# Optimization experiments

Measured on AMD Instinct MI355X. Metric: run time of the kernel, lower is better.

Reference implementation:

```python
import jax, jax.numpy as jnp
import numpy as np
from jax import lax

B, C, OUT, H, W = 8, 512, 512, 64, 64
BN_EPS = 1e-5


def setup_inputs() -> dict:
    key = jax.random.key(0)
    ks = jax.random.split(key, 20)
    s = 1.0 / np.sqrt(C)
    d = {
        "input1": jax.random.normal(ks[0], (B, C, H, W), jnp.float32),
        "input2": jax.random.normal(ks[1], (B, C, H, W), jnp.float32),
        "wq1": jax.random.normal(ks[2], (C, C), jnp.float32) * s,
        "bq1": jnp.zeros((C,), jnp.float32),
        "wk1": jax.random.normal(ks[3], (C, C), jnp.float32) * s,
        "bk1": jnp.zeros((C,), jnp.float32),
        "wv1": jax.random.normal(ks[4], (C, C), jnp.float32) * s,
        "bv1": jnp.zeros((C,), jnp.float32),
        "wq2": jax.random.normal(ks[5], (C, C), jnp.float32) * s,
        "bq2": jnp.zeros((C,), jnp.float32),
        "wk2": jax.random.normal(ks[6], (C, C), jnp.float32) * s,
        "bk2": jnp.zeros((C,), jnp.float32),
        "wv2": jax.random.normal(ks[7], (C, C), jnp.float32) * s,
        "bv2": jnp.zeros((C,), jnp.float32),
        "w_lin": jax.random.normal(ks[8], (1, C), jnp.float32) * s,  # shared gate conv, no bias
        "w_cat": jax.random.normal(ks[9], (OUT, 2 * C, 3, 3), jnp.float32) * (1.0 / np.sqrt(2 * C * 9)),
        "bn_gamma": jnp.ones((OUT,), jnp.float32),
        "bn_beta": jnp.zeros((OUT,), jnp.float32),
    }
    return d


def _conv1x1(x, w, b):
    # x: [B,C,H,W], w: [O,C] -> [B,O,H,W]
    return jnp.einsum('bchw,oc->bohw', x, w) + b[None, :, None, None]


def _branch(x_q_src, x_kv_src, wq, bq, wk, bk, wv, bv, w_lin, x_resid):
    # matches: attn = softmax(k(x_kv) @ q(x_q)^T); out = attn^T @ v(x_kv)
    b, c, h, w = x_kv_src.shape
    n = h * w
    q = _conv1x1(x_q_src, wq, bq).reshape(b, c, n)      # [B,C,N] (from the OTHER input)
    k = _conv1x1(x_kv_src, wk, bk).reshape(b, c, n)
    v = _conv1x1(x_kv_src, wv, bv).reshape(b, c, n)
    attn = jnp.einsum('bkn,bcn->bkc', k, q)             # [B,C,C]
    attn = jax.nn.softmax(attn, axis=-1)
    out = jnp.einsum('bkc,bkn->bcn', attn, v).reshape(b, c, h, w)
    # sigmoid gate: linear(avgpool(x_resid)) -> scalar per batch
    pooled = jnp.mean(x_resid, axis=(2, 3))             # [B,C]
    a = jax.nn.sigmoid(pooled @ w_lin.T)                # [B,1]
    return out * a[:, :, None, None] + x_resid


def reference(input1, input2, wq1, bq1, wk1, bk1, wv1, bv1,
              wq2, bq2, wk2, bk2, wv2, bv2, w_lin, w_cat, bn_gamma, bn_beta):
    # branch 1: k1 from input1, q2 from input2, v1 from input1, gate from input1
    out1 = _branch(input2, input1, wq2, bq2, wk1, bk1, wv1, bv1, w_lin, input1)
    # branch 2: k2 from input2, q1 from input1, v2 from input2, gate from input2
    out2 = _branch(input1, input2, wq1, bq1, wk2, bk2, wv2, bv2, w_lin, input2)
    x = jnp.concatenate([out1, out2], axis=1)           # [B,2C,H,W]
    y = lax.conv_general_dilated(x, w_cat, (1, 1), 'SAME',
                                 dimension_numbers=('NCHW', 'OIHW', 'NCHW'))
    # BatchNorm2d in training mode: batch statistics over (N,H,W)
    mean = jnp.mean(y, axis=(0, 2, 3), keepdims=True)
    var = jnp.var(y, axis=(0, 2, 3), keepdims=True)
    y = (y - mean) * lax.rsqrt(var + BN_EPS)
    y = y * bn_gamma[None, :, None, None] + bn_beta[None, :, None, None]
    return jax.nn.relu(y)
```

## Files before the change

kernel.cpp:

```cpp
#include <hip/hip_runtime.h>


typedef unsigned short u16;
typedef unsigned int u32;
typedef float f32x4 __attribute__((ext_vector_type(4)));
typedef short bf16x8 __attribute__((ext_vector_type(8)));

#define DEV __device__ __forceinline__

DEV u16 f2bf(float f) {
  u32 u = __float_as_uint(f);
  return (u16)((u + 0x7fffu + ((u >> 16) & 1u)) >> 16);
}
DEV float bf2f(u16 u) { return __uint_as_float(((u32)u) << 16); }

DEV void gload_lds16(const void* g, void* l) {
  __builtin_amdgcn_global_load_lds(
      (const __attribute__((address_space(1))) void*)g,
      (__attribute__((address_space(3))) void*)l, 16, 0, 0);
}

DEV void stage_tile(u16* L, const u16* src, int row0, long ld, int k0, int wid, int lane) {
  int rr = lane >> 2;
  int cc = (lane & 3) << 3;
#pragma unroll
  for (int j = 0; j < 2; ++j) {
    int chunk = j * 4 + wid;
    const u16* g = src + (long)(row0 + chunk * 16 + rr) * ld + (k0 + cc);
    gload_lds16(g, L + chunk * 512);
  }
}

DEV float waveRedSum(float v) {
#pragma unroll
  for (int o = 32; o > 0; o >>= 1) v += __shfl_xor(v, o);
  return v;
}

DEV float blockReduceSum256(float v) {
  __shared__ float r[4];
  v = waveRedSum(v);
  int tid = threadIdx.x;
  if ((tid & 63) == 0) r[tid >> 6] = v;
  __syncthreads();
  return r[0] + r[1] + r[2] + r[3];
}

__global__ __launch_bounds__(256) void gemm_gramK(const float* __restrict__ X1,
                                                  const float* __restrict__ X2,
                                                  float* __restrict__ parts)
{
  __shared__ __align__(16) u16 lds[4 * 4096];
  const int bid = blockIdx.x;
  const int cid = ((bid & 7) << 6) + (bid >> 3);
  const int z = cid >> 4, xy = cid & 15;
  const int quarter = z >> 3, b = z & 7;
  const int m0 = (xy & 3) * 128, n0 = (xy >> 2) * 128;
  const int tid = threadIdx.x, wid = tid >> 6, lane = tid & 63;
  const int wr = wid >> 1, wc = wid & 1;
  const int r16 = lane & 15, koff = (lane >> 4) << 3;
  const float* A = X1 + (long)b * 2097152 + quarter * 1024;
  const float* Bp = X2 + (long)b * 2097152 + quarter * 1024;
  const int sr = tid >> 3;
  const int sc = (tid & 7) * 4;

  f32x4 acc[4][4];
#pragma unroll
  for (int i = 0; i < 4; ++i)
#pragma unroll
    for (int j = 0; j < 4; ++j) acc[i][j] = (f32x4){0.f, 0.f, 0.f, 0.f};

  for (int k0 = 0; k0 < 1024; k0 += 32) {
    __syncthreads();
#pragma unroll
    for (int rr = 0; rr < 128; rr += 32) {
      float4 va = *(const float4*)&A[(long)(m0 + rr + sr) * 4096 + k0 + sc];
      float4 vb = *(const float4*)&Bp[(long)(n0 + rr + sr) * 4096 + k0 + sc];
      float fa[4] = {va.x, va.y, va.z, va.w};
      float fb[4] = {vb.x, vb.y, vb.z, vb.w};
      u32 pah0 = 0, pah1 = 0, pal0 = 0, pal1 = 0;
      u32 pbh0 = 0, pbh1 = 0, pbl0 = 0, pbl1 = 0;
#pragma unroll
      for (int e = 0; e < 2; ++e) {
        u16 h = f2bf(fa[e]);      pah0 |= ((u32)h) << (16 * e);
        u16 lo = f2bf(fa[e] - bf2f(h)); pal0 |= ((u32)lo) << (16 * e);
        h = f2bf(fa[e + 2]);      pah1 |= ((u32)h) << (16 * e);
        lo = f2bf(fa[e + 2] - bf2f(h)); pal1 |= ((u32)lo) << (16 * e);
        h = f2bf(fb[e]);          pbh0 |= ((u32)h) << (16 * e);
        lo = f2bf(fb[e] - bf2f(h)); pbl0 |= ((u32)lo) << (16 * e);
        h = f2bf(fb[e + 2]);      pbh1 |= ((u32)h) << (16 * e);
        lo = f2bf(fb[e + 2] - bf2f(h)); pbl1 |= ((u32)lo) << (16 * e);
      }
      int off = (rr + sr) * 32 + sc;
      *(uint2*)&lds[off]         = make_uint2(pah0, pah1);
      *(uint2*)&lds[4096 + off]  = make_uint2(pal0, pal1);
      *(uint2*)&lds[8192 + off]  = make_uint2(pbh0, pbh1);
      *(uint2*)&lds[12288 + off] = make_uint2(pbl0, pbl1);
    }
    __syncthreads();
    bf16x8 ah[4], al[4], bh[4], bl[4];
#pragma unroll
    for (int mi = 0; mi < 4; ++mi) {
      ah[mi] = *(const bf16x8*)&lds[(wr * 64 + mi * 16 + r16) * 32 + koff];
      al[mi] = *(const bf16x8*)&lds[4096 + (wr * 64 + mi * 16 + r16) * 32 + koff];
    }
#pragma unroll
    for (int nj = 0; nj < 4; ++nj) {
      bh[nj] = *(const bf16x8*)&lds[8192 + (wc * 64 + nj * 16 + r16) * 32 + koff];
      bl[nj] = *(const bf16x8*)&lds[12288 + (wc * 64 + nj * 16 + r16) * 32 + koff];
    }
#pragma unroll
    for (int mi = 0; mi < 4; ++mi)
#pragma unroll
      for (int nj = 0; nj < 4; ++nj) {
        acc[mi][nj] = __builtin_amdgcn_mfma_f32_16x16x32_bf16(ah[mi], bh[nj], acc[mi][nj], 0, 0, 0);
        acc[mi][nj] = __builtin_amdgcn_mfma_f32_16x16x32_bf16(ah[mi], bl[nj], acc[mi][nj], 0, 0, 0);
        acc[mi][nj] = __builtin_amdgcn_mfma_f32_16x16x32_bf16(al[mi], bh[nj], acc[mi][nj], 0, 0, 0);
      }
  }

  const int rq = lane >> 4;
  float* O = parts + (long)z * 262144;
#pragma unroll
  for (int mi = 0; mi < 4; ++mi)
#pragma unroll
    for (int nj = 0; nj < 4; ++nj)
#pragma unroll
      for (int i = 0; i < 4; ++i) {
        int row = m0 + wr * 64 + mi * 16 + rq * 4 + i;
        int col = n0 + wc * 64 + nj * 16 + r16;
        O[(long)row * 512 + col] = acc[mi][nj][i];
      }
}

__global__ __launch_bounds__(256) void k_gsplit(const float* __restrict__ parts,
                                                u16* __restrict__ Gh, u16* __restrict__ Gl)
{
  for (long i = (long)blockIdx.x * 256 + threadIdx.x; i < 2097152; i += (long)gridDim.x * 256) {
    float v = parts[i] + parts[i + 2097152] + parts[i + 4194304] + parts[i + 6291456];
    u16 h = f2bf(v);
    Gh[i] = h;
    Gl[i] = f2bf(v - bf2f(h));
  }
}

constexpr int EP_SPLIT = 0, EP_LOGITS = 1, EP_BF16 = 2, EP_XCAT = 3;

struct GArgs {
  const u16* Ah[2]; const u16* Al[2];
  const u16* Bh[2]; const u16* Bl[2];
  long Az[2], Bz[2];
  void* O0[2]; void* O1[2];
  const float* f0[2]; const float* f1[2];
  const float* f2[2]; const float* f3[2];
  const u16* rptr[2];
};

template <int EP, bool SPLIT3, bool FLAT>
__global__ __launch_bounds__(256) void gemm_tn2(GArgs ga, int lda, int ldb, int K, long Oz)
{
  __shared__ __align__(16) u16 lds[(SPLIT3 ? 4 : 2) * 4096];
  int bx, by, z;
  if constexpr (FLAT) {
    const int cid = ((blockIdx.x & 7) << 8) + (blockIdx.x >> 3);
    z = cid >> 7;
    const int xy = cid & 127;
    bx = xy >> 2; by = xy & 3;
  } else {
    bx = blockIdx.x; by = blockIdx.y; z = blockIdx.z;
  }
  const int br = z >> 3, b = z & 7;
  const u16* pAh = ga.Ah[br] + (long)b * ga.Az[br];
  const u16* pBh = ga.Bh[br] + (long)b * ga.Bz[br];
  const u16* pAl = SPLIT3 ? ga.Al[br] + (long)b * ga.Az[br] : nullptr;
  const u16* pBl = SPLIT3 ? ga.Bl[br] + (long)b * ga.Bz[br] : nullptr;
  const int m0 = bx * 128, n0 = by * 128;
  const int tid = threadIdx.x, wid = tid >> 6, lane = tid & 63;
  const int wr = wid >> 1, wc = wid & 1;
  const int r16 = lane & 15, koff = (lane >> 4) << 3;

  f32x4 acc[4][4];
#pragma unroll
  for (int i = 0; i < 4; ++i)
#pragma unroll
    for (int j = 0; j < 4; ++j) acc[i][j] = (f32x4){0.f, 0.f, 0.f, 0.f};

  for (int k0 = 0; k0 < K; k0 += 32) {
    __syncthreads();
    stage_tile(lds, pAh, m0, lda, k0, wid, lane);
    stage_tile(lds + 4096, pBh, n0, ldb, k0, wid, lane);
    if constexpr (SPLIT3) {
      stage_tile(lds + 8192, pAl, m0, lda, k0, wid, lane);
      stage_tile(lds + 12288, pBl, n0, ldb, k0, wid, lane);
    }
    __syncthreads();
    bf16x8 af[4], bfh[4], af2[4], bf2_[4];
#pragma unroll
    for (int mi = 0; mi < 4; ++mi)
      af[mi] = *(const bf16x8*)&lds[(wr * 64 + mi * 16 + r16) * 32 + koff];
#pragma unroll
    for (int nj = 0; nj < 4; ++nj)
      bfh[nj] = *(const bf16x8*)&lds[4096 + (wc * 64 + nj * 16 + r16) * 32 + koff];
    if constexpr (SPLIT3) {
#pragma unroll
      for (int mi = 0; mi < 4; ++mi)
        af2[mi] = *(const bf16x8*)&lds[8192 + (wr * 64 + mi * 16 + r16) * 32 + koff];
#pragma unroll
      for (int nj = 0; nj < 4; ++nj)
        bf2_[nj] = *(const bf16x8*)&lds[12288 + (wc * 64 + nj * 16 + r16) * 32 + koff];
    }
#pragma unroll
    for (int mi = 0; mi < 4; ++mi)
#pragma unroll
      for (int nj = 0; nj < 4; ++nj) {
        acc[mi][nj] = __builtin_amdgcn_mfma_f32_16x16x32_bf16(af[mi], bfh[nj], acc[mi][nj], 0, 0, 0);
        if constexpr (SPLIT3) {
          acc[mi][nj] = __builtin_amdgcn_mfma_f32_16x16x32_bf16(af[mi], bf2_[nj], acc[mi][nj], 0, 0, 0);
          acc[mi][nj] = __builtin_amdgcn_mfma_f32_16x16x32_bf16(af2[mi], bfh[nj], acc[mi][nj], 0, 0, 0);
        }
      }
  }

  const int rq = lane >> 4;
  const long off = (long)z * Oz;
  float g = 0.f;
  if constexpr (EP == EP_XCAT) g = ga.f1[br][b];
#pragma unroll
  for (int mi = 0; mi < 4; ++mi)
#pragma unroll
    for (int nj = 0; nj < 4; ++nj)
#pragma unroll
      for (int i = 0; i < 4; ++i) {
        int row = m0 + wr * 64 + mi * 16 + rq * 4 + i;
        int col = n0 + wc * 64 + nj * 16 + r16;
        float v = acc[mi][nj][i];
        if constexpr (EP == EP_SPLIT) {
          long idx = off + (long)row * 512 + col;
          u16 h = f2bf(v);
          ((u16*)ga.O0[br])[idx] = h;
          ((u16*)ga.O1[br])[idx] = f2bf(v - bf2f(h));
        } else if constexpr (EP == EP_LOGITS) {
          v += ga.f0[br][row] * ga.f3[br][b * 512 + col] + ga.f1[br][col] * ga.f2[br][b * 512 + row];
          ((float*)ga.O0[br])[off + (long)row * 512 + col] = v;
        } else if constexpr (EP == EP_BF16) {
          ((u16*)ga.O0[br])[off + (long)row * 512 + col] = f2bf(v);
        } else {
          float val = (v + ga.f0[br][b * 512 + col]) * g +
                      bf2f(ga.rptr[br][(long)b * 2097152 + (long)row * 512 + col]);
          int yy = row >> 6, xx = row & 63;
          long oidx = ((long)(b * 66 + yy + 1) * 66 + (xx + 1)) * 512 + col;
          ((u16*)ga.O0[br])[oidx] = f2bf(val);
        }
      }
}

#define MF(a, b, c) __builtin_amdgcn_mfma_f32_16x16x32_bf16(a, b, c, 0, 0, 0)
#define SCHEDB() __builtin_amdgcn_sched_barrier(0)
#define BAR() __builtin_amdgcn_s_barrier()
#define STG_B(QB, i) gload_lds16(xb + sbo[i] + kko, &lds[(QB) + ldsB0 + (i) * 4096])
#define STG_A(QB, i) gload_lds16(Arow + (i) * 294912L + Aoff, &lds[(QB) + ldsA0 + (i) * 2048])

#define RD_A(d, fmb)                                                        \
  d##0 = *(const bf16x8*)&lds[pBase + aRd + (fmb) * 1024 + sxa0];           \
  d##1 = *(const bf16x8*)&lds[pBase + aRd + (fmb) * 1024 + sxa1];           \
  d##2 = *(const bf16x8*)&lds[pBase + aRd + ((fmb) + 1) * 1024 + sxa0];     \
  d##3 = *(const bf16x8*)&lds[pBase + aRd + ((fmb) + 1) * 1024 + sxa1];

#define MM(jj, r)                                                           \
  __builtin_amdgcn_s_setprio(1);                                            \
  _Pragma("unroll")                                                         \
  for (int fn = 0; fn < 4; ++fn) {                                          \
    acc[2 * (jj)][fn] = MF(r##0, bq[fn][0], acc[2 * (jj)][fn]);             \
    acc[2 * (jj)][fn] = MF(r##1, bq[fn][1], acc[2 * (jj)][fn]);             \
    acc[2 * (jj) + 1][fn] = MF(r##2, bq[fn][0], acc[2 * (jj) + 1][fn]);     \
    acc[2 * (jj) + 1][fn] = MF(r##3, bq[fn][1], acc[2 * (jj) + 1][fn]);     \
  }                                                                         \
  __builtin_amdgcn_s_setprio(0);                                            \
  SCHEDB();

__global__ __launch_bounds__(512, 2) void k_conv8(const u16* __restrict__ W,
                                                  const u16* __restrict__ xA,
                                                  const u16* __restrict__ xB,
                                                  float* __restrict__ y,
                                                  float* __restrict__ bnsum,
                                                  float* __restrict__ bnsum2)
{
  __shared__ __align__(16) u16 lds[65536];
  const int cid = ((blockIdx.x & 7) << 5) + (blockIdx.x >> 3);
  const int bz = cid >> 5, mx = (cid >> 4) & 1, ny = cid & 15;
  const int m0 = mx * 256, n0 = ny * 256;
  const long zoff = (long)bz * 2230272;

  const int tid = threadIdx.x;
  const int w = tid >> 6, l = tid & 63;
  const int wr = w >> 2, wcn = w & 3, wl = w & 3;
  const int lr = l >> 3, l7 = l & 7, l15 = l & 15, l4 = l >> 4;
  const int ss8 = (l7 ^ lr) << 3;

  long sbo[4];
#pragma unroll
  for (int i = 0; i < 4; ++i) {
    int n = n0 + i * 64 + w * 8 + lr;
    sbo[i] = (long)((n >> 6) * 66 + (n & 63)) * 512;
  }
  const u16* Arow = W + (long)(m0 + wr * 128 + wl * 8 + lr) * 9216 + ss8;
  const int ldsA0 = wr * 8192 + wl * 512;
  const int ldsB0 = 16384 + w * 512;
  const int sxa0 = (l4 ^ l7) << 3;
  const int sxa1 = ((l4 | 4) ^ l7) << 3;
  const int aRd = wr * 8192 + l15 * 64;
  const int bRd = 16384 + wcn * 4096 + l15 * 64;

  f32x4 acc[8][4];
#pragma unroll
  for (int i = 0; i < 8; ++i)
#pragma unroll
    for (int j = 0; j < 4; ++j) acc[i][j] = (f32x4){0.f, 0.f, 0.f, 0.f};

  {
    const u16* xb = xA + zoff;
    const long kko = ss8;
    const long Aoff = 0;
    STG_B(0, 0); STG_B(0, 1); STG_B(0, 2); STG_B(0, 3);
    STG_A(0, 0); STG_A(0, 1); STG_A(0, 2); STG_A(0, 3);
  }

  for (int t = 0; t < 144; ++t) {
    const int pBase = (t & 1) << 15;
    const int qBase = pBase ^ 32768;
    const int tau = t + 1;
    const bool pf = tau < 144;
    const int ccc = tau / 9;
    const int tap = tau - ccc * 9;
    const int cch = ccc << 6;
    const u16* xb = ((cch & 512) ? xB : xA) + zoff;
    const long kko = (long)((tap / 3) * 66 + (tap % 3)) * 512 + (cch & 511) + ss8;
    const long Aoff = (long)(tap << 10) + cch;
    bf16x8 bq[4][2];
    bf16x8 cA0, cA1, cA2, cA3, nA0, nA1, nA2, nA3;

    if (pf) { STG_B(qBase, 0); STG_B(qBase, 1); asm volatile("s_waitcnt vmcnt(4)" ::: "memory"); }
    else    { asm volatile("s_waitcnt vmcnt(2)" ::: "memory"); }
    BAR(); SCHEDB();
#pragma unroll
    for (int fn = 0; fn < 4; ++fn) {
      bq[fn][0] = *(const bf16x8*)&lds[pBase + bRd + fn * 1024 + sxa0];
      bq[fn][1] = *(const bf16x8*)&lds[pBase + bRd + fn * 1024 + sxa1];
    }
    RD_A(cA, 0)
    RD_A(nA, 2)
    SCHEDB();
    MM(0, cA)
    if (pf) { STG_B(qBase, 2); STG_B(qBase, 3); asm volatile("s_waitcnt vmcnt(5)" ::: "memory"); }
    else    { asm volatile("s_waitcnt vmcnt(1)" ::: "memory"); }
    BAR(); SCHEDB();
    RD_A(cA, 4)
    SCHEDB();
    MM(1, nA)
    if (pf) { STG_A(qBase, 0); STG_A(qBase, 1); asm volatile("s_waitcnt vmcnt(6)" ::: "memory"); }
    else    { asm volatile("s_waitcnt vmcnt(0)" ::: "memory"); }
    BAR(); SCHEDB();
    RD_A(nA, 6)
    SCHEDB();
    MM(2, cA)
    if (pf) { STG_A(qBase, 2); STG_A(qBase, 3); }
    BAR(); SCHEDB();
    MM(3, nA)
  }

#pragma unroll
  for (int fm = 0; fm < 8; ++fm)
#pragma unroll
    for (int fn = 0; fn < 4; ++fn)
#pragma unroll
      for (int i = 0; i < 4; ++i) {
        int row = m0 + wr * 128 + fm * 16 + l4 * 4 + i;
        int col = n0 + wcn * 64 + fn * 16 + l15;
        y[((long)bz * 512 + row) * 4096 + col] = acc[fm][fn][i];
      }

  __syncthreads();
  float* fl = (float*)lds;
#pragma unroll
  for (int fm = 0; fm < 8; ++fm)
#pragma unroll
    for (int i = 0; i < 4; ++i) {
      float s = acc[fm][0][i] + acc[fm][1][i] + acc[fm][2][i] + acc[fm][3][i];
      float s2 = acc[fm][0][i] * acc[fm][0][i] + acc[fm][1][i] * acc[fm][1][i] +
                 acc[fm][2][i] * acc[fm][2][i] + acc[fm][3][i] * acc[fm][3][i];
#pragma unroll
      for (int m = 1; m < 16; m <<= 1) { s += __shfl_xor(s, m); s2 += __shfl_xor(s2, m); }
      if (l15 == 0) {
        int r = wr * 128 + fm * 16 + l4 * 4 + i;
        fl[r * 4 + wcn] = s;
        fl[1024 + r * 4 + wcn] = s2;
      }
    }
  __syncthreads();
  {
    int r = tid & 255;
    int which = tid >> 8;
    const float* p = fl + which * 1024 + r * 4;
    float v = p[0] + p[1] + p[2] + p[3];
    atomicAdd((which ? bnsum2 : bnsum) + m0 + r, v);
  }
}

__global__ __launch_bounds__(256) void k_border(u16* __restrict__ xcat, float* __restrict__ rsum,
                                                float* __restrict__ bnsum)
{
  const long base = (long)blockIdx.x * 2230272;
  const int tid = threadIdx.x;
  const uint4 z4 = make_uint4(0, 0, 0, 0);
  for (int i = tid; i < 8448; i += 256) {
    long off = (i < 4224) ? (long)i * 8 : (long)65 * 66 * 512 + (long)(i - 4224) * 8;
    *(uint4*)&xcat[base + off] = z4;
  }
  for (int i = tid; i < 8192; i += 256) {
    int y = 1 + (i >> 7);
    int xsel = (i >> 6) & 1;
    int v = i & 63;
    long off = ((long)y * 66 + (xsel ? 65 : 0)) * 512 + (long)v * 8;
    *(uint4*)&xcat[base + off] = z4;
  }
  float4 f4 = {0.f, 0.f, 0.f, 0.f};
  if (blockIdx.x == 0) {
    for (int i = tid; i < 2048; i += 256) ((float4*)rsum)[i] = f4;
  } else if (blockIdx.x == 1) {
    for (int i = tid; i < 256; i += 256) ((float4*)bnsum)[i] = f4;
  }
}

__global__ __launch_bounds__(256) void k_prep(const float* __restrict__ src,
                                              u16* __restrict__ xT, float* __restrict__ rsum)
{
  __shared__ float t[64][65];
  const int b = blockIdx.z, cb = blockIdx.y, nb = blockIdx.x;
  const float* s = src + (long)b * 2097152;
  const int tid = threadIdx.x;
#pragma unroll
  for (int it = 0; it < 4; ++it) {
    int cr = it * 16 + (tid >> 4);
    int nc = (tid & 15) * 4;
    float4 v = *(const float4*)&s[(long)(cb * 64 + cr) * 4096 + nb * 64 + nc];
    t[cr][nc] = v.x; t[cr][nc + 1] = v.y; t[cr][nc + 2] = v.z; t[cr][nc + 3] = v.w;
  }
  __syncthreads();
  int nr = tid >> 2, cs = (tid & 3) * 16;
  u16 hh[16] __attribute__((aligned(16)));
#pragma unroll
  for (int j = 0; j < 16; ++j) hh[j] = f2bf(t[cs + j][nr]);
  long d = (long)b * 2097152 + (long)(nb * 64 + nr) * 512 + cb * 64 + cs;
  *(uint4*)&xT[d] = *(const uint4*)&hh[0];
  *(uint4*)&xT[d + 8] = *(const uint4*)&hh[8];
  if (tid < 64) {
    float sum = 0.f;
#pragma unroll 8
    for (int j = 0; j < 64; ++j) sum += t[tid][j];
    atomicAdd(&rsum[b * 512 + cb * 64 + tid], sum);
  }
}

__global__ __launch_bounds__(256) void k_tr(const float* __restrict__ src, u16* __restrict__ dst,
                                            int scols, int srows, long zsrc, long zdst)
{
  __shared__ float t[64][65];
  src += (long)blockIdx.z * zsrc;
  dst += (long)blockIdx.z * zdst;
  const int c0 = blockIdx.x * 64, r0 = blockIdx.y * 64;
  const int tid = threadIdx.x;
#pragma unroll
  for (int it = 0; it < 4; ++it) {
    int rr = it * 16 + (tid >> 4);
    int cc = (tid & 15) * 4;
    float4 v = *(const float4*)&src[(long)(r0 + rr) * scols + c0 + cc];
    t[rr][cc] = v.x; t[rr][cc + 1] = v.y; t[rr][cc + 2] = v.z; t[rr][cc + 3] = v.w;
  }
  __syncthreads();
  int nr = tid >> 2, cs = (tid & 3) * 16;
  u16 hh[16] __attribute__((aligned(16)));
#pragma unroll
  for (int j = 0; j < 16; ++j) hh[j] = f2bf(t[cs + j][nr]);
  long d = (long)(c0 + nr) * srows + r0 + cs;
  *(uint4*)&dst[d] = *(const uint4*)&hh[0];
  *(uint4*)&dst[d + 8] = *(const uint4*)&hh[8];
}

__global__ __launch_bounds__(256) void k_gate(const float* __restrict__ rowsum,
                                              const float* __restrict__ wlin,
                                              float* __restrict__ gates)
{
  int id = blockIdx.x;
  int inp = id >> 3, b = id & 7;
  int tid = threadIdx.x;
  float s = 0.f;
  for (int c = tid; c < 512; c += 256) s += rowsum[inp * 4096 + b * 512 + c] * wlin[c];
  s = blockReduceSum256(s);
  if (tid == 0) gates[id] = 1.f / (1.f + __expf(-s / 4096.f));
}

__global__ __launch_bounds__(256) void k_skq(const float* __restrict__ wk1, const float* __restrict__ wq2,
                                             const float* __restrict__ wk2, const float* __restrict__ wq1,
                                             const float* __restrict__ bq2, const float* __restrict__ bq1,
                                             const float* __restrict__ rowsum, float* __restrict__ S)
{
  int which = blockIdx.y, b = blockIdx.z;
  int row = blockIdx.x * 4 + (threadIdx.x >> 6);
  int lane = threadIdx.x & 63;
  const float* W; const float* rs; const float* bias = nullptr;
  if (which == 0)      { W = wk1; rs = rowsum + b * 512; }
  else if (which == 1) { W = wq2; rs = rowsum + 4096 + b * 512; bias = bq2; }
  else if (which == 2) { W = wk2; rs = rowsum + 4096 + b * 512; }
  else                 { W = wq1; rs = rowsum + b * 512; bias = bq1; }
  float s = 0.f;
  for (int i = lane; i < 512; i += 64) s += W[row * 512 + i] * rs[i];
  s = waveRedSum(s);
  if (lane == 0) S[(which * 8 + b) * 512 + row] = s + (bias ? 4096.f * bias[row] : 0.f);
}

__global__ __launch_bounds__(256) void k_mbias(const u16* __restrict__ attnT,
                                               const float* __restrict__ bv1,
                                               const float* __restrict__ bv2,
                                               float* __restrict__ mb)
{
  int z = blockIdx.y;
  int c = blockIdx.x * 4 + (threadIdx.x >> 6);
  int lane = threadIdx.x & 63;
  const float* bv = (z >= 8) ? bv2 : bv1;
  const u16* row = attnT + (long)z * 262144 + (long)c * 512;
  float s = 0.f;
  for (int k = lane; k < 512; k += 64) s += bf2f(row[k]) * bv[k];
  s = waveRedSum(s);
  if (lane == 0) mb[z * 512 + c] = s;
}

struct SplitArgs { const float* s[4]; u16* h[4]; u16* l[4]; };
__global__ __launch_bounds__(256) void k_split4(SplitArgs a)
{
  int which = blockIdx.x >> 8;
  const float* s = a.s[which];
  u16* h = a.h[which];
  u16* l = a.l[which];
  for (int i = (blockIdx.x & 255) * 256 + threadIdx.x; i < 262144; i += 65536) {
    float v = s[i];
    u16 hh = f2bf(v);
    h[i] = hh;
    l[i] = f2bf(v - bf2f(hh));
  }
}

__global__ __launch_bounds__(256) void k_wcat(const float* __restrict__ src, u16* __restrict__ dst)
{
  __shared__ float t[9 * 1029];
  const int o = blockIdx.x;
  const int tid = threadIdx.x;
  const float* s = src + (long)o * 9216;
#pragma unroll
  for (int it = 0; it < 9; ++it) {
    int f4 = it * 256 + tid;
    float4 v = *(const float4*)&s[f4 * 4];
    float va[4] = {v.x, v.y, v.z, v.w};
    int f = f4 * 4;
#pragma unroll
    for (int e = 0; e < 4; ++e) {
      int ic = (f + e) / 9, tp = (f + e) - ic * 9;
      t[tp * 1029 + ic] = va[e];
    }
  }
  __syncthreads();
  u16* d = dst + (long)o * 9216;
#pragma unroll
  for (int tp = 0; tp < 9; ++tp)
#pragma unroll
    for (int c = 0; c < 4; ++c) {
      int ic = c * 256 + tid;
      d[tp * 1024 + ic] = f2bf(t[tp * 1029 + ic]);
    }
}

__global__ __launch_bounds__(256) void k_softmaxT(const float* __restrict__ L,
                                                  u16* __restrict__ attnT)
{
  const int bid = blockIdx.x;
  const int z = bid >> 4, rg = bid & 15;
  const int w = threadIdx.x >> 6, lane = threadIdx.x & 63;
  const int a0 = rg * 32 + w * 8;
  const float* Lz = L + (long)z * 262144;
  u16* Az = attnT + (long)z * 262144;
  u32 pk[8][4] = {};
#pragma unroll
  for (int it = 0; it < 8; ++it) {
    long base = (long)(a0 + it) * 512 + lane * 8;
    float4 p0 = *(const float4*)&Lz[base], p1 = *(const float4*)&Lz[base + 4];
    float v[8] = {p0.x, p0.y, p0.z, p0.w, p1.x, p1.y, p1.z, p1.w};
    float m = v[0];
#pragma unroll
    for (int j = 1; j < 8; ++j) m = fmaxf(m, v[j]);
#pragma unroll
    for (int o = 32; o > 0; o >>= 1) m = fmaxf(m, __shfl_xor(m, o));
    float e[8], s = 0.f;
#pragma unroll
    for (int j = 0; j < 8; ++j) { e[j] = __expf(v[j] - m); s += e[j]; }
    s = waveRedSum(s);
    float inv = 1.f / s;
#pragma unroll
    for (int j = 0; j < 8; ++j)
      pk[j][it >> 1] |= ((u32)f2bf(e[j] * inv)) << ((it & 1) * 16);
  }
#pragma unroll
  for (int j = 0; j < 8; ++j) {
    int c = lane * 8 + j;
    *(uint4*)&Az[(long)c * 512 + a0] = make_uint4(pk[j][0], pk[j][1], pk[j][2], pk[j][3]);
  }
}

__global__ __launch_bounds__(512) void k_bnstat(const float* __restrict__ bnsum,
                                                const float* __restrict__ bnsum2,
                                                const float* __restrict__ gamma,
                                                const float* __restrict__ beta,
                                                float* __restrict__ sc, float* __restrict__ sh)
{
  int o = threadIdx.x;
  float mean = bnsum[o] / 32768.f;
  float var = bnsum2[o] / 32768.f - mean * mean;
  float rstd = rsqrtf(var + 1e-5f);
  float scale = gamma[o] * rstd;
  sc[o] = scale;
  sh[o] = beta[o] - mean * scale;
}

__global__ __launch_bounds__(256) void k_bnapply(float* __restrict__ y,
                                                 const float* __restrict__ sc,
                                                 const float* __restrict__ sh)
{
  const long n = 16777216;
  for (long i = ((long)blockIdx.x * 256 + threadIdx.x) * 4; i < n; i += (long)gridDim.x * 1024) {
    float4 v = *(const float4*)&y[i];
    int o = (int)((i >> 12) & 511);
    float a = sc[o], c = sh[o];
    v.x = fmaxf(v.x * a + c, 0.f);
    v.y = fmaxf(v.y * a + c, 0.f);
    v.z = fmaxf(v.z * a + c, 0.f);
    v.w = fmaxf(v.w * a + c, 0.f);
    *(float4*)&y[i] = v;
  }
}

extern "C" void kernel_launch(void* const* d_in, const int* in_sizes, int n_in,
                              void* d_out, int out_size, void* d_ws, size_t ws_size,
                              hipStream_t stream)
{
  (void)in_sizes; (void)n_in; (void)out_size; (void)ws_size;
  const float* in1 = (const float*)d_in[0];
  const float* in2 = (const float*)d_in[1];
  const float* wq1 = (const float*)d_in[2];  const float* bq1 = (const float*)d_in[3];
  const float* wk1 = (const float*)d_in[4];  const float* bk1 = (const float*)d_in[5];
  const float* wv1 = (const float*)d_in[6];  const float* bv1 = (const float*)d_in[7];
  const float* wq2 = (const float*)d_in[8];  const float* bq2 = (const float*)d_in[9];
  const float* wk2 = (const float*)d_in[10]; const float* bk2 = (const float*)d_in[11];
  const float* wv2 = (const float*)d_in[12]; const float* bv2 = (const float*)d_in[13];
  const float* wlin  = (const float*)d_in[14];
  const float* wcat  = (const float*)d_in[15];
  const float* gamma = (const float*)d_in[16];
  const float* beta  = (const float*)d_in[17];

  char* ws = (char*)d_ws;
  const size_t MB = 1024ull * 1024ull;
  u16* Gh     = (u16*)(ws + 0 * MB);
  u16* Gl     = (u16*)(ws + 4 * MB);
  u16* Mb     = (u16*)(ws + 0 * MB);
  u16* Uh     = (u16*)(ws + 8 * MB);
  u16* attnT  = (u16*)(ws + 8 * MB);
  u16* Ul     = (u16*)(ws + 16 * MB);
  float* logits = (float*)(ws + 24 * MB);
  float* parts  = (float*)(ws + 8 * MB);
  u16* xcatA  = (u16*)(ws + 40 * MB);
  u16* xcatB  = xcatA + 8L * 2230272;
  u16* wcp    = (u16*)(ws + 112 * MB);
  u16* wsp    = (u16*)(ws + 122 * MB);
  u16* WvT1   = (u16*)(ws + 126 * MB);
  u16* WvT2   = WvT1 + 262144;
  float* rowsum = (float*)(ws + 127 * MB);
  float* gates  = (float*)(ws + 127 * MB + 32 * 1024);
  float* S      = (float*)(ws + 127 * MB + 36 * 1024);
  float* mb     = (float*)(ws + 127 * MB + 100 * 1024);
  float* bnsum  = (float*)(ws + 127 * MB + 132 * 1024);
  float* bnsum2 = (float*)(ws + 127 * MB + 134 * 1024);
  float* bnsc   = (float*)(ws + 127 * MB + 136 * 1024);
  float* bnsh   = (float*)(ws + 127 * MB + 138 * 1024);

  u16* wq1h = wsp + 0 * 262144; u16* wq1l = wsp + 1 * 262144;
  u16* wq2h = wsp + 2 * 262144; u16* wq2l = wsp + 3 * 262144;
  u16* wk1h = wsp + 4 * 262144; u16* wk1l = wsp + 5 * 262144;
  u16* wk2h = wsp + 6 * 262144; u16* wk2l = wsp + 7 * 262144;

  u16* xT1 = (u16*)d_out;
  u16* xT2 = (u16*)d_out + 16777216;
  float* ybuf = (float*)d_out;

  k_border<<<16, 256, 0, stream>>>(xcatA, rowsum, bnsum);
  k_prep<<<dim3(64, 8, 8), 256, 0, stream>>>(in1, xT1, rowsum);
  k_prep<<<dim3(64, 8, 8), 256, 0, stream>>>(in2, xT2, rowsum + 4096);
  k_tr<<<dim3(8, 8, 1), 256, 0, stream>>>(wv1, WvT1, 512, 512, 0L, 0L);
  k_tr<<<dim3(8, 8, 1), 256, 0, stream>>>(wv2, WvT2, 512, 512, 0L, 0L);
  {
    SplitArgs sa;
    sa.s[0] = wq1; sa.h[0] = wq1h; sa.l[0] = wq1l;
    sa.s[1] = wq2; sa.h[1] = wq2h; sa.l[1] = wq2l;
    sa.s[2] = wk1; sa.h[2] = wk1h; sa.l[2] = wk1l;
    sa.s[3] = wk2; sa.h[3] = wk2h; sa.l[3] = wk2l;
    k_split4<<<1024, 256, 0, stream>>>(sa);
  }
  k_wcat<<<512, 256, 0, stream>>>(wcat, wcp);
  k_gate<<<16, 256, 0, stream>>>(rowsum, wlin, gates);
  k_skq<<<dim3(128, 4, 8), 256, 0, stream>>>(wk1, wq2, wk2, wq1, bq2, bq1, rowsum, S);

  gemm_gramK<<<512, 256, 0, stream>>>(in1, in2, parts);
  k_gsplit<<<2048, 256, 0, stream>>>(parts, Gh, Gl);

  {
    GArgs ga = {};
    ga.Ah[0] = wq2h; ga.Al[0] = wq2l; ga.Ah[1] = wk2h; ga.Al[1] = wk2l;
    ga.Az[0] = 0; ga.Az[1] = 0;
    ga.Bh[0] = Gh; ga.Bl[0] = Gl; ga.Bh[1] = Gh; ga.Bl[1] = Gl;
    ga.Bz[0] = 262144; ga.Bz[1] = 262144;
    ga.O0[0] = Uh; ga.O0[1] = Uh; ga.O1[0] = Ul; ga.O1[1] = Ul;
    gemm_tn2<EP_SPLIT, true, false><<<dim3(4, 4, 16), 256, 0, stream>>>(ga, 512, 512, 512, 262144);
  }
  {
    GArgs ga = {};
    ga.Ah[0] = wk1h; ga.Al[0] = wk1l; ga.Az[0] = 0;
    ga.Ah[1] = Uh + 2097152; ga.Al[1] = Ul + 2097152; ga.Az[1] = 262144;
    ga.Bh[0] = Uh; ga.Bl[0] = Ul; ga.Bz[0] = 262144;
    ga.Bh[1] = wq1h; ga.Bl[1] = wq1l; ga.Bz[1] = 0;
    ga.O0[0] = logits; ga.O0[1] = logits;
    ga.f0[0] = bk1; ga.f1[0] = bq2; ga.f2[0] = S;        ga.f3[0] = S + 4096;
    ga.f0[1] = bk2; ga.f1[1] = bq1; ga.f2[1] = S + 8192; ga.f3[1] = S + 12288;
    gemm_tn2<EP_LOGITS, true, false><<<dim3(4, 4, 16), 256, 0, stream>>>(ga, 512, 512, 512, 262144);
  }
  k_softmaxT<<<256, 256, 0, stream>>>(logits, attnT);
  k_mbias<<<dim3(128, 16), 256, 0, stream>>>(attnT, bv1, bv2, mb);
  {
    GArgs ga = {};
    ga.Ah[0] = attnT; ga.Ah[1] = attnT + 2097152;
    ga.Az[0] = 262144; ga.Az[1] = 262144;
    ga.Bh[0] = WvT1; ga.Bh[1] = WvT2; ga.Bz[0] = 0; ga.Bz[1] = 0;
    ga.O0[0] = Mb; ga.O0[1] = Mb;
    gemm_tn2<EP_BF16, false, false><<<dim3(4, 4, 16), 256, 0, stream>>>(ga, 512, 512, 512, 262144);
  }
  {
    GArgs ga = {};
    ga.Ah[0] = xT1; ga.Ah[1] = xT2; ga.Az[0] = 2097152; ga.Az[1] = 2097152;
    ga.Bh[0] = Mb; ga.Bh[1] = Mb + 2097152; ga.Bz[0] = 262144; ga.Bz[1] = 262144;
    ga.O0[0] = xcatA; ga.O0[1] = xcatB;
    ga.f0[0] = mb; ga.f0[1] = mb + 4096;
    ga.f1[0] = gates; ga.f1[1] = gates + 8;
    ga.rptr[0] = xT1; ga.rptr[1] = xT2;
    gemm_tn2<EP_XCAT, false, true><<<2048, 256, 0, stream>>>(ga, 512, 512, 512, 0);
  }

  k_conv8<<<256, 512, 0, stream>>>(wcp, xcatA, xcatB, ybuf, bnsum, bnsum2);
  k_bnstat<<<1, 512, 0, stream>>>(bnsum, bnsum2, gamma, beta, bnsc, bnsh);
  k_bnapply<<<4096, 256, 0, stream>>>(ybuf, bnsc, bnsh);
}
```

Baseline: 613.6 us.

## Merge small prep, gate, mbias and BN-stat kernels to cut launches

Several small setup kernels (border zeroing, Wv transpose, weight split, wcat repack, accumulator zeroing) are merged into one multi-role kernel, and the two input prep launches become one. The gate goes into k_skq, the mbias reduction into softmax through atomics, and BN scale/shift is recomputed inside bnapply. Some SCHEDB barriers are also dropped from the conv loop. This removes about seven launches and their serialization gaps, at the cost of atomics in softmax and redundant per-element BN stat math.

Result: faster. 601.2 us (-2.0%).

```diff
diff --git a/kernel.cpp b/kernel.cpp
--- a/kernel.cpp
+++ b/kernel.cpp
@@ -35,15 +35,6 @@
 #pragma unroll
   for (int o = 32; o > 0; o >>= 1) v += __shfl_xor(v, o);
   return v;
-}
-
-DEV float blockReduceSum256(float v) {
-  __shared__ float r[4];
-  v = waveRedSum(v);
-  int tid = threadIdx.x;
-  if ((tid & 63) == 0) r[tid >> 6] = v;
-  __syncthreads();
-  return r[0] + r[1] + r[2] + r[3];
 }
 
 __global__ __launch_bounds__(256) void gemm_gramK(const float* __restrict__ X1,
@@ -349,19 +340,16 @@
     }
     RD_A(cA, 0)
     RD_A(nA, 2)
-    SCHEDB();
     MM(0, cA)
     if (pf) { STG_B(qBase, 2); STG_B(qBase, 3); asm volatile("s_waitcnt vmcnt(5)" ::: "memory"); }
     else    { asm volatile("s_waitcnt vmcnt(1)" ::: "memory"); }
     BAR(); SCHEDB();
     RD_A(cA, 4)
-    SCHEDB();
     MM(1, nA)
     if (pf) { STG_A(qBase, 0); STG_A(qBase, 1); asm volatile("s_waitcnt vmcnt(6)" ::: "memory"); }
     else    { asm volatile("s_waitcnt vmcnt(0)" ::: "memory"); }
     BAR(); SCHEDB();
     RD_A(nA, 6)
-    SCHEDB();
     MM(2, cA)
     if (pf) { STG_A(qBase, 2); STG_A(qBase, 3); }
     BAR(); SCHEDB();
@@ -406,37 +394,110 @@
   }
 }
 
-__global__ __launch_bounds__(256) void k_border(u16* __restrict__ xcat, float* __restrict__ rsum,
-                                                float* __restrict__ bnsum)
-{
-  const long base = (long)blockIdx.x * 2230272;
+struct PrepArgs {
+  const float* wv1; const float* wv2;
+  u16* WvT1; u16* WvT2;
+  const float* s[4]; u16* h[4]; u16* l[4];
+  const float* wcat; u16* wcp;
+  u16* xcat;
+  float* rsum; float* bnsum; float* mbz;
+};
+
+__global__ __launch_bounds__(256) void k_mprep(PrepArgs a)
+{
+  __shared__ __align__(16) float shbuf[9261];
+  const int bx = blockIdx.x;
   const int tid = threadIdx.x;
-  const uint4 z4 = make_uint4(0, 0, 0, 0);
-  for (int i = tid; i < 8448; i += 256) {
-    long off = (i < 4224) ? (long)i * 8 : (long)65 * 66 * 512 + (long)(i - 4224) * 8;
-    *(uint4*)&xcat[base + off] = z4;
-  }
-  for (int i = tid; i < 8192; i += 256) {
-    int y = 1 + (i >> 7);
-    int xsel = (i >> 6) & 1;
-    int v = i & 63;
-    long off = ((long)y * 66 + (xsel ? 65 : 0)) * 512 + (long)v * 8;
-    *(uint4*)&xcat[base + off] = z4;
-  }
-  float4 f4 = {0.f, 0.f, 0.f, 0.f};
-  if (blockIdx.x == 0) {
-    for (int i = tid; i < 2048; i += 256) ((float4*)rsum)[i] = f4;
-  } else if (blockIdx.x == 1) {
-    for (int i = tid; i < 256; i += 256) ((float4*)bnsum)[i] = f4;
-  }
-}
-
-__global__ __launch_bounds__(256) void k_prep(const float* __restrict__ src,
-                                              u16* __restrict__ xT, float* __restrict__ rsum)
+  if (bx < 128) {
+    const float* src = (bx < 64) ? a.wv1 : a.wv2;
+    u16* dst = (bx < 64) ? a.WvT1 : a.WvT2;
+    const int t8 = bx & 63;
+    const int c0 = (t8 & 7) * 64, r0 = (t8 >> 3) * 64;
+#pragma unroll
+    for (int it = 0; it < 4; ++it) {
+      int rr = it * 16 + (tid >> 4);
+      int cc = (tid & 15) * 4;
+      float4 v = *(const float4*)&src[(long)(r0 + rr) * 512 + c0 + cc];
+      shbuf[rr * 65 + cc] = v.x; shbuf[rr * 65 + cc + 1] = v.y;
+      shbuf[rr * 65 + cc + 2] = v.z; shbuf[rr * 65 + cc + 3] = v.w;
+    }
+    __syncthreads();
+    int nr = tid >> 2, cs = (tid & 3) * 16;
+    u16 hh[16] __attribute__((aligned(16)));
+#pragma unroll
+    for (int j = 0; j < 16; ++j) hh[j] = f2bf(shbuf[(cs + j) * 65 + nr]);
+    long d = (long)(c0 + nr) * 512 + r0 + cs;
+    *(uint4*)&dst[d] = *(const uint4*)&hh[0];
+    *(uint4*)&dst[d + 8] = *(const uint4*)&hh[8];
+  } else if (bx < 1152) {
+    int which = (bx - 128) >> 8;
+    const float* s = a.s[which];
+    u16* h = a.h[which];
+    u16* l = a.l[which];
+    for (int i = ((bx - 128) & 255) * 256 + tid; i < 262144; i += 65536) {
+      float v = s[i];
+      u16 hh = f2bf(v);
+      h[i] = hh;
+      l[i] = f2bf(v - bf2f(hh));
+    }
+  } else if (bx < 1664) {
+    const int o = bx - 1152;
+    const float* s = a.wcat + (long)o * 9216;
+#pragma unroll
+    for (int it = 0; it < 9; ++it) {
+      int f4 = it * 256 + tid;
+      float4 v = *(const float4*)&s[f4 * 4];
+      float va[4] = {v.x, v.y, v.z, v.w};
+      int f = f4 * 4;
+#pragma unroll
+      for (int e = 0; e < 4; ++e) {
+        int ic = (f + e) / 9, tp = (f + e) - ic * 9;
+        shbuf[tp * 1029 + ic] = va[e];
+      }
+    }
+    __syncthreads();
+    u16* d = a.wcp + (long)o * 9216;
+#pragma unroll
+    for (int tp = 0; tp < 9; ++tp)
+#pragma unroll
+      for (int c = 0; c < 4; ++c) {
+        int ic = c * 256 + tid;
+        d[tp * 1024 + ic] = f2bf(shbuf[tp * 1029 + ic]);
+      }
+  } else if (bx < 1680) {
+    const long base = (long)(bx - 1664) * 2230272;
+    const uint4 z4 = make_uint4(0, 0, 0, 0);
+    for (int i = tid; i < 8448; i += 256) {
+      long off = (i < 4224) ? (long)i * 8 : (long)65 * 66 * 512 + (long)(i - 4224) * 8;
+      *(uint4*)&a.xcat[base + off] = z4;
+    }
+    for (int i = tid; i < 8192; i += 256) {
+      int y = 1 + (i >> 7);
+      int xsel = (i >> 6) & 1;
+      int v = i & 63;
+      long off = ((long)y * 66 + (xsel ? 65 : 0)) * 512 + (long)v * 8;
+      *(uint4*)&a.xcat[base + off] = z4;
+    }
+  } else {
+    float4 f4 = {0.f, 0.f, 0.f, 0.f};
+    for (int i = tid; i < 2048; i += 256) ((float4*)a.rsum)[i] = f4;
+    for (int i = tid; i < 256; i += 256) ((float4*)a.bnsum)[i] = f4;
+    for (int i = tid; i < 2048; i += 256) ((float4*)a.mbz)[i] = f4;
+  }
+}
+
+__global__ __launch_bounds__(256) void k_prep(const float* __restrict__ in1,
+                                              const float* __restrict__ in2,
+                                              u16* __restrict__ xT1, u16* __restrict__ xT2,
+                                              float* __restrict__ rsum)
 {
   __shared__ float t[64][65];
-  const int b = blockIdx.z, cb = blockIdx.y, nb = blockIdx.x;
-  const float* s = src + (long)b * 2097152;
+  const int zz = blockIdx.z;
+  const int inp = zz >> 3, b = zz & 7;
+  const int cb = blockIdx.y, nb = blockIdx.x;
+  const float* s = (inp ? in2 : in1) + (long)b * 2097152;
+  u16* xT = inp ? xT2 : xT1;
+  float* rs = rsum + inp * 4096;
   const int tid = threadIdx.x;
 #pragma unroll
   for (int it = 0; it < 4; ++it) {
@@ -457,56 +518,30 @@
     float sum = 0.f;
 #pragma unroll 8
     for (int j = 0; j < 64; ++j) sum += t[tid][j];
-    atomicAdd(&rsum[b * 512 + cb * 64 + tid], sum);
-  }
-}
-
-__global__ __launch_bounds__(256) void k_tr(const float* __restrict__ src, u16* __restrict__ dst,
-                                            int scols, int srows, long zsrc, long zdst)
-{
-  __shared__ float t[64][65];
-  src += (long)blockIdx.z * zsrc;
-  dst += (long)blockIdx.z * zdst;
-  const int c0 = blockIdx.x * 64, r0 = blockIdx.y * 64;
-  const int tid = threadIdx.x;
-#pragma unroll
-  for (int it = 0; it < 4; ++it) {
-    int rr = it * 16 + (tid >> 4);
-    int cc = (tid & 15) * 4;
-    float4 v = *(const float4*)&src[(long)(r0 + rr) * scols + c0 + cc];
-    t[rr][cc] = v.x; t[rr][cc + 1] = v.y; t[rr][cc + 2] = v.z; t[rr][cc + 3] = v.w;
-  }
-  __syncthreads();
-  int nr = tid >> 2, cs = (tid & 3) * 16;
-  u16 hh[16] __attribute__((aligned(16)));
-#pragma unroll
-  for (int j = 0; j < 16; ++j) hh[j] = f2bf(t[cs + j][nr]);
-  long d = (long)(c0 + nr) * srows + r0 + cs;
-  *(uint4*)&dst[d] = *(const uint4*)&hh[0];
-  *(uint4*)&dst[d + 8] = *(const uint4*)&hh[8];
-}
-
-__global__ __launch_bounds__(256) void k_gate(const float* __restrict__ rowsum,
-                                              const float* __restrict__ wlin,
-                                              float* __restrict__ gates)
-{
-  int id = blockIdx.x;
-  int inp = id >> 3, b = id & 7;
-  int tid = threadIdx.x;
-  float s = 0.f;
-  for (int c = tid; c < 512; c += 256) s += rowsum[inp * 4096 + b * 512 + c] * wlin[c];
-  s = blockReduceSum256(s);
-  if (tid == 0) gates[id] = 1.f / (1.f + __expf(-s / 4096.f));
+    atomicAdd(&rs[b * 512 + tid + cb * 64], sum);
+  }
 }
 
 __global__ __launch_bounds__(256) void k_skq(const float* __restrict__ wk1, const float* __restrict__ wq2,
                                              const float* __restrict__ wk2, const float* __restrict__ wq1,
                                              const float* __restrict__ bq2, const float* __restrict__ bq1,
-                                             const float* __restrict__ rowsum, float* __restrict__ S)
+                                             const float* __restrict__ wlin,
+                                             const float* __restrict__ rowsum,
+                                             float* __restrict__ S, float* __restrict__ gates)
 {
   int which = blockIdx.y, b = blockIdx.z;
+  int lane = threadIdx.x & 63;
+  if (which == 4) {
+    if (blockIdx.x < 2 && threadIdx.x < 64) {
+      int inp = blockIdx.x;
+      float s = 0.f;
+      for (int c = lane; c < 512; c += 64) s += rowsum[inp * 4096 + b * 512 + c] * wlin[c];
+      s = waveRedSum(s);
+      if (lane == 0) gates[inp * 8 + b] = 1.f / (1.f + __expf(-s / 4096.f));
+    }
+    return;
+  }
   int row = blockIdx.x * 4 + (threadIdx.x >> 6);
-  int lane = threadIdx.x & 63;
   const float* W; const float* rs; const float* bias = nullptr;
   if (which == 0)      { W = wk1; rs = rowsum + b * 512; }
   else if (which == 1) { W = wq2; rs = rowsum + 4096 + b * 512; bias = bq2; }
@@ -518,76 +553,21 @@
   if (lane == 0) S[(which * 8 + b) * 512 + row] = s + (bias ? 4096.f * bias[row] : 0.f);
 }
 
-__global__ __launch_bounds__(256) void k_mbias(const u16* __restrict__ attnT,
-                                               const float* __restrict__ bv1,
-                                               const float* __restrict__ bv2,
-                                               float* __restrict__ mb)
-{
-  int z = blockIdx.y;
-  int c = blockIdx.x * 4 + (threadIdx.x >> 6);
-  int lane = threadIdx.x & 63;
-  const float* bv = (z >= 8) ? bv2 : bv1;
-  const u16* row = attnT + (long)z * 262144 + (long)c * 512;
-  float s = 0.f;
-  for (int k = lane; k < 512; k += 64) s += bf2f(row[k]) * bv[k];
-  s = waveRedSum(s);
-  if (lane == 0) mb[z * 512 + c] = s;
-}
-
-struct SplitArgs { const float* s[4]; u16* h[4]; u16* l[4]; };
-__global__ __launch_bounds__(256) void k_split4(SplitArgs a)
-{
-  int which = blockIdx.x >> 8;
-  const float* s = a.s[which];
-  u16* h = a.h[which];
-  u16* l = a.l[which];
-  for (int i = (blockIdx.x & 255) * 256 + threadIdx.x; i < 262144; i += 65536) {
-    float v = s[i];
-    u16 hh = f2bf(v);
-    h[i] = hh;
-    l[i] = f2bf(v - bf2f(hh));
-  }
-}
-
-__global__ __launch_bounds__(256) void k_wcat(const float* __restrict__ src, u16* __restrict__ dst)
-{
-  __shared__ float t[9 * 1029];
-  const int o = blockIdx.x;
-  const int tid = threadIdx.x;
-  const float* s = src + (long)o * 9216;
-#pragma unroll
-  for (int it = 0; it < 9; ++it) {
-    int f4 = it * 256 + tid;
-    float4 v = *(const float4*)&s[f4 * 4];
-    float va[4] = {v.x, v.y, v.z, v.w};
-    int f = f4 * 4;
-#pragma unroll
-    for (int e = 0; e < 4; ++e) {
-      int ic = (f + e) / 9, tp = (f + e) - ic * 9;
-      t[tp * 1029 + ic] = va[e];
-    }
-  }
-  __syncthreads();
-  u16* d = dst + (long)o * 9216;
-#pragma unroll
-  for (int tp = 0; tp < 9; ++tp)
-#pragma unroll
-    for (int c = 0; c < 4; ++c) {
-      int ic = c * 256 + tid;
-      d[tp * 1024 + ic] = f2bf(t[tp * 1029 + ic]);
-    }
-}
-
 __global__ __launch_bounds__(256) void k_softmaxT(const float* __restrict__ L,
-                                                  u16* __restrict__ attnT)
+                                                  u16* __restrict__ attnT,
+                                                  const float* __restrict__ bv1,
+                                                  const float* __restrict__ bv2,
+                                                  float* __restrict__ mb)
 {
   const int bid = blockIdx.x;
   const int z = bid >> 4, rg = bid & 15;
   const int w = threadIdx.x >> 6, lane = threadIdx.x & 63;
   const int a0 = rg * 32 + w * 8;
   const float* Lz = L + (long)z * 262144;
+  const float* bv = (z >= 8) ? bv2 : bv1;
   u16* Az = attnT + (long)z * 262144;
   u32 pk[8][4] = {};
+  float pmb[8] = {};
 #pragma unroll
   for (int it = 0; it < 8; ++it) {
     long base = (long)(a0 + it) * 512 + lane * 8;
@@ -603,41 +583,36 @@
     for (int j = 0; j < 8; ++j) { e[j] = __expf(v[j] - m); s += e[j]; }
     s = waveRedSum(s);
     float inv = 1.f / s;
-#pragma unroll
-    for (int j = 0; j < 8; ++j)
-      pk[j][it >> 1] |= ((u32)f2bf(e[j] * inv)) << ((it & 1) * 16);
+    float bvv = bv[a0 + it];
+#pragma unroll
+    for (int j = 0; j < 8; ++j) {
+      float p = e[j] * inv;
+      pk[j][it >> 1] |= ((u32)f2bf(p)) << ((it & 1) * 16);
+      pmb[j] += p * bvv;
+    }
   }
 #pragma unroll
   for (int j = 0; j < 8; ++j) {
     int c = lane * 8 + j;
     *(uint4*)&Az[(long)c * 512 + a0] = make_uint4(pk[j][0], pk[j][1], pk[j][2], pk[j][3]);
-  }
-}
-
-__global__ __launch_bounds__(512) void k_bnstat(const float* __restrict__ bnsum,
-                                                const float* __restrict__ bnsum2,
-                                                const float* __restrict__ gamma,
-                                                const float* __restrict__ beta,
-                                                float* __restrict__ sc, float* __restrict__ sh)
-{
-  int o = threadIdx.x;
-  float mean = bnsum[o] / 32768.f;
-  float var = bnsum2[o] / 32768.f - mean * mean;
-  float rstd = rsqrtf(var + 1e-5f);
-  float scale = gamma[o] * rstd;
-  sc[o] = scale;
-  sh[o] = beta[o] - mean * scale;
+    atomicAdd(&mb[z * 512 + c], pmb[j]);
+  }
 }
 
 __global__ __launch_bounds__(256) void k_bnapply(float* __restrict__ y,
-                                                 const float* __restrict__ sc,
-                                                 const float* __restrict__ sh)
+                                                 const float* __restrict__ bnsum,
+                                                 const float* __restrict__ bnsum2,
+                                                 const float* __restrict__ gamma,
+                                                 const float* __restrict__ beta)
 {
   const long n = 16777216;
   for (long i = ((long)blockIdx.x * 256 + threadIdx.x) * 4; i < n; i += (long)gridDim.x * 1024) {
     float4 v = *(const float4*)&y[i];
     int o = (int)((i >> 12) & 511);
-    float a = sc[o], c = sh[o];
+    float mean = bnsum[o] * (1.f / 32768.f);
+    float var = bnsum2[o] * (1.f / 32768.f) - mean * mean;
+    float a = gamma[o] * rsqrtf(var + 1e-5f);
+    float c = beta[o] - mean * a;
     v.x = fmaxf(v.x * a + c, 0.f);
     v.y = fmaxf(v.y * a + c, 0.f);
     v.z = fmaxf(v.z * a + c, 0.f);
@@ -686,8 +661,6 @@
   float* mb     = (float*)(ws + 127 * MB + 100 * 1024);
   float* bnsum  = (float*)(ws + 127 * MB + 132 * 1024);
   float* bnsum2 = (float*)(ws + 127 * MB + 134 * 1024);
-  float* bnsc   = (float*)(ws + 127 * MB + 136 * 1024);
-  float* bnsh   = (float*)(ws + 127 * MB + 138 * 1024);
 
   u16* wq1h = wsp + 0 * 262144; u16* wq1l = wsp + 1 * 262144;
   u16* wq2h = wsp + 2 * 262144; u16* wq2l = wsp + 3 * 262144;
@@ -698,22 +671,20 @@
   u16* xT2 = (u16*)d_out + 16777216;
   float* ybuf = (float*)d_out;
 
-  k_border<<<16, 256, 0, stream>>>(xcatA, rowsum, bnsum);
-  k_prep<<<dim3(64, 8, 8), 256, 0, stream>>>(in1, xT1, rowsum);
-  k_prep<<<dim3(64, 8, 8), 256, 0, stream>>>(in2, xT2, rowsum + 4096);
-  k_tr<<<dim3(8, 8, 1), 256, 0, stream>>>(wv1, WvT1, 512, 512, 0L, 0L);
-  k_tr<<<dim3(8, 8, 1), 256, 0, stream>>>(wv2, WvT2, 512, 512, 0L, 0L);
   {
-    SplitArgs sa;
-    sa.s[0] = wq1; sa.h[0] = wq1h; sa.l[0] = wq1l;
-    sa.s[1] = wq2; sa.h[1] = wq2h; sa.l[1] = wq2l;
-    sa.s[2] = wk1; sa.h[2] = wk1h; sa.l[2] = wk1l;
-    sa.s[3] = wk2; sa.h[3] = wk2h; sa.l[3] = wk2l;
-    k_split4<<<1024, 256, 0, stream>>>(sa);
-  }
-  k_wcat<<<512, 256, 0, stream>>>(wcat, wcp);
-  k_gate<<<16, 256, 0, stream>>>(rowsum, wlin, gates);
-  k_skq<<<dim3(128, 4, 8), 256, 0, stream>>>(wk1, wq2, wk2, wq1, bq2, bq1, rowsum, S);
+    PrepArgs pa;
+    pa.wv1 = wv1; pa.wv2 = wv2; pa.WvT1 = WvT1; pa.WvT2 = WvT2;
+    pa.s[0] = wq1; pa.h[0] = wq1h; pa.l[0] = wq1l;
+    pa.s[1] = wq2; pa.h[1] = wq2h; pa.l[1] = wq2l;
+    pa.s[2] = wk1; pa.h[2] = wk1h; pa.l[2] = wk1l;
+    pa.s[3] = wk2; pa.h[3] = wk2h; pa.l[3] = wk2l;
+    pa.wcat = wcat; pa.wcp = wcp;
+    pa.xcat = xcatA;
+    pa.rsum = rowsum; pa.bnsum = bnsum; pa.mbz = mb;
+    k_mprep<<<1681, 256, 0, stream>>>(pa);
+  }
+  k_prep<<<dim3(64, 8, 16), 256, 0, stream>>>(in1, in2, xT1, xT2, rowsum);
+  k_skq<<<dim3(128, 5, 8), 256, 0, stream>>>(wk1, wq2, wk2, wq1, bq2, bq1, wlin, rowsum, S, gates);
 
   gemm_gramK<<<512, 256, 0, stream>>>(in1, in2, parts);
   k_gsplit<<<2048, 256, 0, stream>>>(parts, Gh, Gl);
@@ -738,8 +709,7 @@
     ga.f0[1] = bk2; ga.f1[1] = bq1; ga.f2[1] = S + 8192; ga.f3[1] = S + 12288;
     gemm_tn2<EP_LOGITS, true, false><<<dim3(4, 4, 16), 256, 0, stream>>>(ga, 512, 512, 512, 262144);
   }
-  k_softmaxT<<<256, 256, 0, stream>>>(logits, attnT);
-  k_mbias<<<dim3(128, 16), 256, 0, stream>>>(attnT, bv1, bv2, mb);
+  k_softmaxT<<<256, 256, 0, stream>>>(logits, attnT, bv1, bv2, mb);
   {
     GArgs ga = {};
     ga.Ah[0] = attnT; ga.Ah[1] = attnT + 2097152;
@@ -760,6 +730,5 @@
   }
 
   k_conv8<<<256, 512, 0, stream>>>(wcp, xcatA, xcatB, ybuf, bnsum, bnsum2);
-  k_bnstat<<<1, 512, 0, stream>>>(bnsum, bnsum2, gamma, beta, bnsc, bnsh);
-  k_bnapply<<<4096, 256, 0, stream>>>(ybuf, bnsc, bnsh);
-}
+  k_bnapply<<<4096, 256, 0, stream>>>(ybuf, bnsum, bnsum2, gamma, beta);
+}
```
